# Performance work log

Hardware: AMD Instinct MI355X
Metric: run time of the kernel (lower is better)

Reference implementation:

```python
import jax, jax.numpy as jnp
import numpy as np

N_NODES = 100000
N_EDGES = 1600000
DIM = 64


def setup_inputs() -> dict:
    key = jax.random.key(0)
    ks = jax.random.split(key, 10)
    return {
        "h_real": jax.random.normal(ks[0], (N_NODES, DIM), dtype=jnp.float32),
        "h_imag": jax.random.normal(ks[1], (N_NODES, DIM), dtype=jnp.float32),
        "d": jax.random.uniform(ks[2], (N_NODES,), dtype=jnp.float32),
        "w_real": jax.random.normal(ks[3], (N_EDGES,), dtype=jnp.float32),
        "w_imag": jax.random.normal(ks[4], (N_EDGES,), dtype=jnp.float32),
        "src": jax.random.randint(ks[5], (N_EDGES,), 0, N_NODES, dtype=jnp.int32),
        "dst": jax.random.randint(ks[6], (N_EDGES,), 0, N_NODES, dtype=jnp.int32),
        "W1": jax.random.normal(ks[7], (DIM, DIM), dtype=jnp.float32) * (1.414 / np.sqrt(DIM)),
        "b1": jnp.zeros((DIM,), dtype=jnp.float32),
        "W2": jax.random.normal(ks[8], (DIM, DIM), dtype=jnp.float32) * (1.414 / np.sqrt(DIM)),
        "b2": jnp.zeros((DIM,), dtype=jnp.float32),
    }


def reference(h_real, h_imag, d, w_real, w_imag, src, dst, W1, b1, W2, b2):
    n = h_real.shape[0]
    # per-edge complex coefficient e = d_dst * d_src * (w_real + i w_imag)
    dd = d[dst] * d[src]                      # [E]
    e_r = (dd * w_real)[:, None]              # [E,1]
    e_i = (dd * w_imag)[:, None]              # [E,1]
    hr = h_real[src]                          # [E,D]
    hi = h_imag[src]                          # [E,D]
    # complex multiply e * h, fused single pass over edges
    m_r = e_r * hr - e_i * hi                 # [E,D]
    m_i = e_i * hr + e_r * hi                 # [E,D]
    z_real = jax.ops.segment_sum(m_r, dst, num_segments=n)  # [N,D]
    z_imag = jax.ops.segment_sum(m_i, dst, num_segments=n)  # [N,D]
    # note: original overwrites z_real first, then z_imag uses the NEW z_real
    zr = (z_real @ W1.T + b1) - (z_imag @ W2.T + b2)
    zi = (zr @ W2.T + b2) + (z_imag @ W1.T + b1)
    return zr, zi
```

## Files before the change

kernel.cpp:

```cpp
#include <hip/hip_runtime.h>
#include <hip/hip_bf16.h>

#define N_NODES 100000
#define N_EDGES 1600000
#define DIM 64

#define TILE 4096
#define B1 ((N_EDGES + TILE - 1) / TILE)
#define K1 ((N_NODES + 255) / 256)
#define NCOUNTS (K1 * B1)
#define SCAN_BLOCK 1024
#define NSB ((NCOUNTS + SCAN_BLOCK - 1) / SCAN_BLOCK)
#define PACKB4 ((N_NODES * DIM / 4 + 255) / 256)
#define QCAP 1344

typedef __attribute__((ext_vector_type(8))) short bf16x8;
typedef __attribute__((ext_vector_type(4))) float f32x4;

#if defined(__has_builtin)
#if __has_builtin(__builtin_amdgcn_fdot2_f32_bf16)
#define HAVE_DOT2 1
typedef __attribute__((ext_vector_type(2))) __bf16 bf16x2v;
#endif
#endif


__device__ __forceinline__ unsigned pack_bf16x2(float lo, float hi) {
  unsigned ulo = (unsigned)__hip_bfloat16_raw(__float2bfloat16(lo)).x;
  unsigned uhi = (unsigned)__hip_bfloat16_raw(__float2bfloat16(hi)).x;
  return ulo | (uhi << 16);
}
__device__ __forceinline__ float unpack_lo(unsigned u) {
  return __int_as_float((int)(u << 16));
}
__device__ __forceinline__ float unpack_hi(unsigned u) {
  return __int_as_float((int)(u & 0xFFFF0000u));
}
__device__ __forceinline__ unsigned short f2bf(float x) {
  return __hip_bfloat16_raw(__float2bfloat16(x)).x;
}

__global__ __launch_bounds__(256) void setup_fused_kernel(
    const float* __restrict__ h_real, const float* __restrict__ h_imag,
    unsigned* __restrict__ hpack, const float* __restrict__ W1,
    const float* __restrict__ b1, const float* __restrict__ W2,
    const float* __restrict__ b2, unsigned short* __restrict__ At,
    float* __restrict__ cvec, const int* __restrict__ dst,
    int* __restrict__ counts) {
  const int bid = blockIdx.x;
  const int tid = threadIdx.x;
  if (bid < PACKB4) {
    const int i = bid * 256 + tid;
    const float4 hr = ((const float4*)h_real)[i];
    const float4 hi = ((const float4*)h_imag)[i];
    uint4 o;
    o.x = pack_bf16x2(hr.x, hi.x);
    o.y = pack_bf16x2(hr.y, hi.y);
    o.z = pack_bf16x2(hr.z, hi.z);
    o.w = pack_bf16x2(hr.w, hi.w);
    ((uint4*)hpack)[i] = o;
    return;
  }
  if (bid < PACKB4 + 64) {
    const int idx = (bid - PACKB4) * 256 + tid;
    if (idx < 128 * 128) {
      const int n = idx >> 7, k = idx & 127;
      float v;
      if (n < 64) {
        v = (k < 64) ? W1[n * 64 + k] : -W2[n * 64 + (k - 64)];
      } else {
        const int nn = n - 64;
        if (k < 64) {
          float s = 0.0f;
          for (int j = 0; j < 64; ++j) s += W1[j * 64 + k] * W2[nn * 64 + j];
          v = s;
        } else {
          const int kk = k - 64;
          float s = 0.0f;
          for (int j = 0; j < 64; ++j) s += W2[j * 64 + kk] * W2[nn * 64 + j];
          v = W1[nn * 64 + kk] - s;
        }
      }
      At[n * 128 + k] = f2bf(v);
    }
    if (idx < 128) {
      if (idx < 64) {
        cvec[idx] = b1[idx] - b2[idx];
      } else {
        const int nn = idx - 64;
        float s = 0.0f;
        for (int j = 0; j < 64; ++j) s += (b1[j] - b2[j]) * W2[nn * 64 + j];
        cvec[idx] = s + b1[nn] + b2[nn];
      }
    }
    return;
  }
  __shared__ int lh[K1];
  const int hb = bid - PACKB4 - 64;
  for (int i = tid; i < K1; i += 256) lh[i] = 0;
  __syncthreads();
  const int e0 = hb * TILE;
  const int e1 = min(e0 + TILE, N_EDGES);
  for (int e = e0 + tid; e < e1; e += 256) atomicAdd(&lh[dst[e] >> 8], 1);
  __syncthreads();
  for (int b = tid; b < K1; b += 256) counts[b * B1 + hb] = lh[b];
}

__global__ __launch_bounds__(SCAN_BLOCK) void scan1_kernel(
    int* __restrict__ cnt, int* __restrict__ bsum) {
  __shared__ int wsum[16];
  const int tid = threadIdx.x;
  const int lane = tid & 63;
  const int w = tid >> 6;
  const int i = blockIdx.x * SCAN_BLOCK + tid;
  const int orig = (i < NCOUNTS) ? cnt[i] : 0;
  int v = orig;
#pragma unroll
  for (int off = 1; off < 64; off <<= 1) {
    int t = __shfl_up(v, off);
    if (lane >= off) v += t;
  }
  if (lane == 63) wsum[w] = v;
  __syncthreads();
  if (w == 0) {
    int s = (lane < 16) ? wsum[lane] : 0;
#pragma unroll
    for (int off = 1; off < 16; off <<= 1) {
      int t = __shfl_up(s, off);
      if (lane >= off) s += t;
    }
    if (lane < 16) wsum[lane] = s;
  }
  __syncthreads();
  const int wex = (w == 0) ? 0 : wsum[w - 1];
  if (i < NCOUNTS) cnt[i] = wex + v - orig;
  if (tid == SCAN_BLOCK - 1) bsum[blockIdx.x] = wex + v;
}

__global__ __launch_bounds__(256) void scan2_kernel(
    const int* __restrict__ bsum, int* __restrict__ bpre) {
  __shared__ int wsum[4];
  const int tid = threadIdx.x;
  const int lane = tid & 63;
  const int w = tid >> 6;
  const int orig = (tid < NSB) ? bsum[tid] : 0;
  int v = orig;
#pragma unroll
  for (int off = 1; off < 64; off <<= 1) {
    int t = __shfl_up(v, off);
    if (lane >= off) v += t;
  }
  if (lane == 63) wsum[w] = v;
  __syncthreads();
  if (w == 0) {
    int s = (lane < 4) ? wsum[lane] : 0;
#pragma unroll
    for (int off = 1; off < 4; off <<= 1) {
      int t = __shfl_up(s, off);
      if (lane >= off) s += t;
    }
    if (lane < 4) wsum[lane] = s;
  }
  __syncthreads();
  const int wex = (w == 0) ? 0 : wsum[w - 1];
  if (tid < NSB) bpre[tid] = wex + v - orig;
}

__global__ __launch_bounds__(512) void partition_kernel(
    const int* __restrict__ src, const int* __restrict__ dst,
    const float* __restrict__ dvec,
    const float* __restrict__ w_real, const float* __restrict__ w_imag,
    const int* __restrict__ coffs, const int* __restrict__ bpre,
    unsigned long long* __restrict__ records) {
  __shared__ unsigned long long stage[TILE];
  __shared__ unsigned short sb[TILE];
  __shared__ int lhist[512];
  __shared__ int lbase[K1];
  __shared__ int lcur[K1];
  __shared__ int gbase[K1];
  __shared__ int wsum[8];
  const int tid = threadIdx.x;
  const int lane = tid & 63;
  const int w = tid >> 6;
  const int blk = blockIdx.x;
  const int e0 = blk * TILE;
  const int cnt_t = min(TILE, N_EDGES - e0);

  lhist[tid] = 0;
  __syncthreads();
  for (int j = tid; j < cnt_t; j += 512) atomicAdd(&lhist[dst[e0 + j] >> 8], 1);
  __syncthreads();
  const int myc = lhist[tid];
  int v = myc;
#pragma unroll
  for (int off = 1; off < 64; off <<= 1) {
    int t = __shfl_up(v, off);
    if (lane >= off) v += t;
  }
  if (lane == 63) wsum[w] = v;
  __syncthreads();
  if (w == 0) {
    int s = (lane < 8) ? wsum[lane] : 0;
#pragma unroll
    for (int off = 1; off < 8; off <<= 1) {
      int t = __shfl_up(s, off);
      if (lane >= off) s += t;
    }
    if (lane < 8) wsum[lane] = s;
  }
  __syncthreads();
  const int ex = v + ((w == 0) ? 0 : wsum[w - 1]) - myc;
  if (tid < K1) {
    lbase[tid] = ex;
    lcur[tid] = ex;
    const int ci = tid * B1 + blk;
    gbase[tid] = coffs[ci] + bpre[ci >> 10];
  }
  __syncthreads();

  for (int j = tid; j < cnt_t; j += 512) {
    const int e = e0 + j;
    const int t = dst[e];
    const int s = src[e];
    const int b = t >> 8;
    const float ds = dvec[s];
    const unsigned lo = (unsigned)s | ((unsigned)(t & 255) << 17);
    const unsigned hi = pack_bf16x2(ds * w_real[e], ds * w_imag[e]);
    const int r = atomicAdd(&lcur[b], 1);
    stage[r] = ((unsigned long long)hi << 32) | lo;
    sb[r] = (unsigned short)b;
  }
  __syncthreads();
  for (int i = tid; i < cnt_t; i += 512) {
    const int b = sb[i];
    records[gbase[b] + (i - lbase[b])] = stage[i];
  }
}

__global__ __launch_bounds__(512, 8) void pull_sorted_kernel(
    const unsigned long long* __restrict__ records,
    const int* __restrict__ coffs, const int* __restrict__ bpre,
    const float* __restrict__ dvec, const unsigned* __restrict__ hpack,
    const unsigned short* __restrict__ At, const float* __restrict__ cvec,
    float* __restrict__ zr_out, float* __restrict__ zi_out) {
  __shared__ unsigned long long stageB[QCAP];
  __shared__ __align__(16) unsigned short zs[64][136];
  __shared__ int ncnt[64];
  __shared__ int ncur[64];
  __shared__ int ns[64];
  __shared__ int ne[64];
  const int tid = threadIdx.x;
  const int lane = tid & 63;
  const int wave = tid >> 6;
  const int q4 = lane >> 4;
  const int m16 = lane & 15;
  const int b256 = blockIdx.x >> 2;
  const int qtr = blockIdx.x & 3;
  const int nbase = b256 * 256 + qtr * 64;
  const unsigned* __restrict__ hb = hpack + 4 * m16;

  const int ci0 = b256 * B1;
  const int bstart = coffs[ci0] + bpre[ci0 >> 10];
  int bend;
  if (b256 == K1 - 1) {
    bend = N_EDGES;
  } else {
    const int ci1 = (b256 + 1) * B1;
    bend = coffs[ci1] + bpre[ci1 >> 10];
  }

  if (tid < 64) ncnt[tid] = 0;
  __syncthreads();

  for (int i = bstart + tid; i < bend; i += 512) {
    const unsigned nl = ((unsigned)records[i] >> 17) & 255u;
    if ((int)(nl >> 6) == qtr) atomicAdd(&ncnt[nl & 63], 1);
  }
  __syncthreads();

  if (wave == 0) {
    const int c = ncnt[lane];
    int v = c;
#pragma unroll
    for (int off = 1; off < 64; off <<= 1) {
      int t = __shfl_up(v, off);
      if (lane >= off) v += t;
    }
    ns[lane] = v - c;
    ne[lane] = v;
    ncur[lane] = v - c;
  }
  __syncthreads();

  for (int i = bstart + tid; i < bend; i += 512) {
    const unsigned long long rec = records[i];
    const unsigned nl = ((unsigned)rec >> 17) & 255u;
    if ((int)(nl >> 6) == qtr) {
      const int pos = atomicAdd(&ncur[nl & 63], 1);
      if (pos < QCAP) stageB[pos] = rec;
    }
  }
  __syncthreads();

#if HAVE_DOT2
#define DOT2(acc, w_, h_)                                                   \
  acc = __builtin_amdgcn_fdot2_f32_bf16(__builtin_bit_cast(bf16x2v, (w_)),  \
                                        __builtin_bit_cast(bf16x2v, (h_)),  \
                                        acc, false)
#else
#define DOT2(acc, w_, h_)                                                   \
  {                                                                         \
    const float _wl = unpack_lo(w_), _wh = unpack_hi(w_);                   \
    const float _hl = unpack_lo(h_), _hh = unpack_hi(h_);                   \
    acc += _wl * _hl + _wh * _hh;                                           \
  }
#endif

#define GATH(RR) \
  (*reinterpret_cast<const uint4*>(hb + (size_t)((unsigned)(RR) & 0x1FFFF) * DIM))

#define DOTS(RR, HV)                                                        \
  {                                                                         \
    const unsigned cf = (unsigned)((RR) >> 32);                             \
    const unsigned wneg = cf ^ 0x80000000u;                                 \
    const unsigned wswp = (cf >> 16) | (cf << 16);                          \
    DOT2(sr0, wneg, (HV).x); DOT2(si0, wswp, (HV).x);                       \
    DOT2(sr1, wneg, (HV).y); DOT2(si1, wswp, (HV).y);                       \
    DOT2(sr2, wneg, (HV).z); DOT2(si2, wswp, (HV).z);                       \
    DOT2(sr3, wneg, (HV).w); DOT2(si3, wswp, (HV).w);                       \
  }

  for (int j = 0; j < 8; ++j) {
    const int l = wave * 8 + j;
    const int n = nbase + l;
    if (n >= N_NODES) break;
    const int s = min(ns[l], QCAP);
    const int e = min(ne[l], QCAP);
    const int deg = e - s;

    float sr0 = 0.f, sr1 = 0.f, sr2 = 0.f, sr3 = 0.f;
    float si0 = 0.f, si1 = 0.f, si2 = 0.f, si3 = 0.f;

    int p = s + q4;
    const int nfull = deg >> 2;
    int i = 0;
    for (; i + 4 <= nfull; i += 4) {
      const unsigned long long ra = stageB[p];
      const unsigned long long rb = stageB[p + 4];
      const unsigned long long rc = stageB[p + 8];
      const unsigned long long rd = stageB[p + 12];
      const uint4 ha = GATH(ra);
      const uint4 hbv = GATH(rb);
      const uint4 hc = GATH(rc);
      const uint4 hd = GATH(rd);
      DOTS(ra, ha) DOTS(rb, hbv) DOTS(rc, hc) DOTS(rd, hd)
      p += 16;
    }
    for (; i + 2 <= nfull; i += 2) {
      const unsigned long long ra = stageB[p];
      const unsigned long long rb = stageB[p + 4];
      const uint4 ha = GATH(ra);
      const uint4 hbv = GATH(rb);
      DOTS(ra, ha) DOTS(rb, hbv)
      p += 8;
    }
    if (i < nfull) {
      const unsigned long long ra = stageB[p];
      const uint4 ha = GATH(ra);
      DOTS(ra, ha)
      p += 4;
    }
    if (p < e) {
      const unsigned long long ra = stageB[p];
      const uint4 ha = GATH(ra);
      DOTS(ra, ha)
    }

#define QRED(v)                  \
    v += __shfl_xor(v, 16);      \
    v += __shfl_xor(v, 32);
    QRED(sr0) QRED(sr1) QRED(sr2) QRED(sr3)
    QRED(si0) QRED(si1) QRED(si2) QRED(si3)
#undef QRED

    const float dn = dvec[n];
    if (lane < 16) {
      uint2 rv, iv;
      rv.x = pack_bf16x2(dn * sr0, dn * sr1);
      rv.y = pack_bf16x2(dn * sr2, dn * sr3);
      iv.x = pack_bf16x2(dn * si0, dn * si1);
      iv.y = pack_bf16x2(dn * si2, dn * si3);
      *reinterpret_cast<uint2*>(&zs[l][4 * lane]) = rv;
      *reinterpret_cast<uint2*>(&zs[l][64 + 4 * lane]) = iv;
    }
  }
#undef DOTS
#undef GATH
#undef DOT2
  __syncthreads();

  {
    const int m = lane & 15;
    const int q = lane >> 4;
    const int ft = wave;
#pragma unroll
    for (int g = 0; g < 4; ++g) {
      bf16x8 a[4];
#pragma unroll
      for (int c = 0; c < 4; ++c)
        a[c] = *reinterpret_cast<const bf16x8*>(&zs[g * 16 + m][c * 32 + q * 8]);

      f32x4 acc = (f32x4){0.f, 0.f, 0.f, 0.f};
      const unsigned short* brow = At + (size_t)(ft * 16 + m) * 128 + q * 8;
#pragma unroll
      for (int c = 0; c < 4; ++c) {
        bf16x8 bfrag = *reinterpret_cast<const bf16x8*>(brow + c * 32);
        acc = __builtin_amdgcn_mfma_f32_16x16x32_bf16(a[c], bfrag, acc, 0, 0, 0);
      }

      const int nf = ft * 16 + m;
      const float bias = cvec[nf];
      float* outp = (nf < 64) ? zr_out : zi_out;
      const int nnn = nf & 63;
#pragma unroll
      for (int r = 0; r < 4; ++r) {
        const int node = nbase + g * 16 + q * 4 + r;
        if (node < N_NODES) outp[(size_t)node * 64 + nnn] = acc[r] + bias;
      }
    }
  }
}

extern "C" void kernel_launch(void* const* d_in, const int* in_sizes, int n_in,
                              void* d_out, int out_size, void* d_ws, size_t ws_size,
                              hipStream_t stream) {
  const float* h_real = (const float*)d_in[0];
  const float* h_imag = (const float*)d_in[1];
  const float* dvec   = (const float*)d_in[2];
  const float* w_real = (const float*)d_in[3];
  const float* w_imag = (const float*)d_in[4];
  const int*   src    = (const int*)d_in[5];
  const int*   dst    = (const int*)d_in[6];
  const float* W1     = (const float*)d_in[7];
  const float* b1     = (const float*)d_in[8];
  const float* W2     = (const float*)d_in[9];
  const float* b2     = (const float*)d_in[10];

  char* ws = (char*)d_ws;
  unsigned short* At = (unsigned short*)ws;
  float* cvec = (float*)(ws + 128 * 128 * 2);
  unsigned long long* records = (unsigned long long*)(ws + 33792);
  unsigned* hpack = (unsigned*)(ws + 33792 + (size_t)N_EDGES * 8);
  int* counts = (int*)(ws + 33792 + (size_t)N_EDGES * 8 + (size_t)N_NODES * DIM * 4);
  int* bsum = counts + NCOUNTS;
  int* bpre = bsum + NSB;

  float* zr_out = (float*)d_out;
  float* zi_out = zr_out + (size_t)N_NODES * DIM;

  setup_fused_kernel<<<PACKB4 + 64 + B1, 256, 0, stream>>>(
      h_real, h_imag, (unsigned*)hpack, W1, b1, W2, b2, At, cvec, dst, counts);
  scan1_kernel<<<NSB, SCAN_BLOCK, 0, stream>>>(counts, bsum);
  scan2_kernel<<<1, 256, 0, stream>>>(bsum, bpre);
  partition_kernel<<<B1, 512, 0, stream>>>(src, dst, dvec, w_real, w_imag,
                                           counts, bpre, records);
  pull_sorted_kernel<<<K1 * 4, 512, 0, stream>>>(
      records, counts, bpre, dvec, hpack, At, cvec, zr_out, zi_out);
}
```

Baseline: 247.9 us.

## Replace per-tile count matrix scan with global bucket counters and atomic cursors

```diff
diff --git a/kernel.cpp b/kernel.cpp
--- a/kernel.cpp
+++ b/kernel.cpp
@@ -8,9 +8,6 @@
 #define TILE 4096
 #define B1 ((N_EDGES + TILE - 1) / TILE)
 #define K1 ((N_NODES + 255) / 256)
-#define NCOUNTS (K1 * B1)
-#define SCAN_BLOCK 1024
-#define NSB ((NCOUNTS + SCAN_BLOCK - 1) / SCAN_BLOCK)
 #define PACKB4 ((N_NODES * DIM / 4 + 255) / 256)
 #define QCAP 1344
 
@@ -46,7 +43,7 @@
     const float* __restrict__ b1, const float* __restrict__ W2,
     const float* __restrict__ b2, unsigned short* __restrict__ At,
     float* __restrict__ cvec, const int* __restrict__ dst,
-    int* __restrict__ counts) {
+    int* __restrict__ bcnt) {
   const int bid = blockIdx.x;
   const int tid = threadIdx.x;
   if (bid < PACKB4) {
@@ -62,23 +59,30 @@
     return;
   }
   if (bid < PACKB4 + 64) {
+    __shared__ float w1s[64 * 64];
+    __shared__ float w2s[64 * 64];
+    for (int i = tid; i < 64 * 64; i += 256) {
+      w1s[i] = W1[i];
+      w2s[i] = W2[i];
+    }
+    __syncthreads();
     const int idx = (bid - PACKB4) * 256 + tid;
     if (idx < 128 * 128) {
       const int n = idx >> 7, k = idx & 127;
       float v;
       if (n < 64) {
-        v = (k < 64) ? W1[n * 64 + k] : -W2[n * 64 + (k - 64)];
+        v = (k < 64) ? w1s[n * 64 + k] : -w2s[n * 64 + (k - 64)];
       } else {
         const int nn = n - 64;
         if (k < 64) {
           float s = 0.0f;
-          for (int j = 0; j < 64; ++j) s += W1[j * 64 + k] * W2[nn * 64 + j];
+          for (int j = 0; j < 64; ++j) s += w1s[j * 64 + k] * w2s[nn * 64 + j];
           v = s;
         } else {
           const int kk = k - 64;
           float s = 0.0f;
-          for (int j = 0; j < 64; ++j) s += W2[j * 64 + kk] * W2[nn * 64 + j];
-          v = W1[nn * 64 + kk] - s;
+          for (int j = 0; j < 64; ++j) s += w2s[j * 64 + kk] * w2s[nn * 64 + j];
+          v = w1s[nn * 64 + kk] - s;
         }
       }
       At[n * 128 + k] = f2bf(v);
@@ -89,7 +93,7 @@
       } else {
         const int nn = idx - 64;
         float s = 0.0f;
-        for (int j = 0; j < 64; ++j) s += (b1[j] - b2[j]) * W2[nn * 64 + j];
+        for (int j = 0; j < 64; ++j) s += (b1[j] - b2[j]) * w2s[nn * 64 + j];
         cvec[idx] = s + b1[nn] + b2[nn];
       }
     }
@@ -103,18 +107,19 @@
   const int e1 = min(e0 + TILE, N_EDGES);
   for (int e = e0 + tid; e < e1; e += 256) atomicAdd(&lh[dst[e] >> 8], 1);
   __syncthreads();
-  for (int b = tid; b < K1; b += 256) counts[b * B1 + hb] = lh[b];
-}
-
-__global__ __launch_bounds__(SCAN_BLOCK) void scan1_kernel(
-    int* __restrict__ cnt, int* __restrict__ bsum) {
-  __shared__ int wsum[16];
+  for (int b = tid; b < K1; b += 256)
+    if (lh[b]) atomicAdd(&bcnt[b], lh[b]);
+}
+
+__global__ __launch_bounds__(512) void scanB_kernel(
+    const int* __restrict__ bcnt, int* __restrict__ cursor,
+    int* __restrict__ bbase) {
+  __shared__ int wsum[8];
   const int tid = threadIdx.x;
   const int lane = tid & 63;
   const int w = tid >> 6;
-  const int i = blockIdx.x * SCAN_BLOCK + tid;
-  const int orig = (i < NCOUNTS) ? cnt[i] : 0;
-  int v = orig;
+  const int c = (tid < K1) ? bcnt[tid] : 0;
+  int v = c;
 #pragma unroll
   for (int off = 1; off < 64; off <<= 1) {
     int t = __shfl_up(v, off);
@@ -123,126 +128,92 @@
   if (lane == 63) wsum[w] = v;
   __syncthreads();
   if (w == 0) {
-    int s = (lane < 16) ? wsum[lane] : 0;
-#pragma unroll
-    for (int off = 1; off < 16; off <<= 1) {
+    int s = (lane < 8) ? wsum[lane] : 0;
+#pragma unroll
+    for (int off = 1; off < 8; off <<= 1) {
       int t = __shfl_up(s, off);
       if (lane >= off) s += t;
     }
-    if (lane < 16) wsum[lane] = s;
-  }
-  __syncthreads();
-  const int wex = (w == 0) ? 0 : wsum[w - 1];
-  if (i < NCOUNTS) cnt[i] = wex + v - orig;
-  if (tid == SCAN_BLOCK - 1) bsum[blockIdx.x] = wex + v;
-}
-
-__global__ __launch_bounds__(256) void scan2_kernel(
-    const int* __restrict__ bsum, int* __restrict__ bpre) {
-  __shared__ int wsum[4];
-  const int tid = threadIdx.x;
-  const int lane = tid & 63;
-  const int w = tid >> 6;
-  const int orig = (tid < NSB) ? bsum[tid] : 0;
-  int v = orig;
-#pragma unroll
-  for (int off = 1; off < 64; off <<= 1) {
-    int t = __shfl_up(v, off);
-    if (lane >= off) v += t;
-  }
-  if (lane == 63) wsum[w] = v;
-  __syncthreads();
-  if (w == 0) {
-    int s = (lane < 4) ? wsum[lane] : 0;
-#pragma unroll
-    for (int off = 1; off < 4; off <<= 1) {
-      int t = __shfl_up(s, off);
-      if (lane >= off) s += t;
-    }
-    if (lane < 4) wsum[lane] = s;
-  }
-  __syncthreads();
-  const int wex = (w == 0) ? 0 : wsum[w - 1];
-  if (tid < NSB) bpre[tid] = wex + v - orig;
+    if (lane < 8) wsum[lane] = s;
+  }
+  __syncthreads();
+  const int incl = v + ((w == 0) ? 0 : wsum[w - 1]);
+  const int excl = incl - c;
+  if (tid < K1) {
+    cursor[tid] = excl;
+    bbase[tid] = excl;
+  }
+  if (tid == K1 - 1) bbase[K1] = incl;
 }
 
 __global__ __launch_bounds__(512) void partition_kernel(
     const int* __restrict__ src, const int* __restrict__ dst,
     const float* __restrict__ dvec,
     const float* __restrict__ w_real, const float* __restrict__ w_imag,
-    const int* __restrict__ coffs, const int* __restrict__ bpre,
-    unsigned long long* __restrict__ records) {
-  __shared__ unsigned long long stage[TILE];
-  __shared__ unsigned short sb[TILE];
-  __shared__ int lhist[512];
-  __shared__ int lbase[K1];
-  __shared__ int lcur[K1];
-  __shared__ int gbase[K1];
-  __shared__ int wsum[8];
+    int* __restrict__ cursor, unsigned long long* __restrict__ records) {
+  __shared__ int lh[K1];
+  __shared__ int mybase[K1];
   const int tid = threadIdx.x;
-  const int lane = tid & 63;
-  const int w = tid >> 6;
   const int blk = blockIdx.x;
   const int e0 = blk * TILE;
   const int cnt_t = min(TILE, N_EDGES - e0);
 
-  lhist[tid] = 0;
-  __syncthreads();
-  for (int j = tid; j < cnt_t; j += 512) atomicAdd(&lhist[dst[e0 + j] >> 8], 1);
-  __syncthreads();
-  const int myc = lhist[tid];
-  int v = myc;
-#pragma unroll
-  for (int off = 1; off < 64; off <<= 1) {
-    int t = __shfl_up(v, off);
-    if (lane >= off) v += t;
-  }
-  if (lane == 63) wsum[w] = v;
-  __syncthreads();
-  if (w == 0) {
-    int s = (lane < 8) ? wsum[lane] : 0;
-#pragma unroll
-    for (int off = 1; off < 8; off <<= 1) {
-      int t = __shfl_up(s, off);
-      if (lane >= off) s += t;
-    }
-    if (lane < 8) wsum[lane] = s;
-  }
-  __syncthreads();
-  const int ex = v + ((w == 0) ? 0 : wsum[w - 1]) - myc;
-  if (tid < K1) {
-    lbase[tid] = ex;
-    lcur[tid] = ex;
-    const int ci = tid * B1 + blk;
-    gbase[tid] = coffs[ci] + bpre[ci >> 10];
-  }
-  __syncthreads();
-
-  for (int j = tid; j < cnt_t; j += 512) {
-    const int e = e0 + j;
-    const int t = dst[e];
-    const int s = src[e];
-    const int b = t >> 8;
-    const float ds = dvec[s];
-    const unsigned lo = (unsigned)s | ((unsigned)(t & 255) << 17);
-    const unsigned hi = pack_bf16x2(ds * w_real[e], ds * w_imag[e]);
-    const int r = atomicAdd(&lcur[b], 1);
-    stage[r] = ((unsigned long long)hi << 32) | lo;
-    sb[r] = (unsigned short)b;
-  }
-  __syncthreads();
-  for (int i = tid; i < cnt_t; i += 512) {
-    const int b = sb[i];
-    records[gbase[b] + (i - lbase[b])] = stage[i];
+  for (int i = tid; i < K1; i += 512) lh[i] = 0;
+  __syncthreads();
+
+#pragma unroll
+  for (int g = 0; g < TILE / 2048; ++g) {
+    const int off = g * 2048 + tid * 4;
+    if (off < cnt_t) {
+      const int4 t4 = *(const int4*)(dst + e0 + off);
+      atomicAdd(&lh[t4.x >> 8], 1);
+      atomicAdd(&lh[t4.y >> 8], 1);
+      atomicAdd(&lh[t4.z >> 8], 1);
+      atomicAdd(&lh[t4.w >> 8], 1);
+    }
+  }
+  __syncthreads();
+
+  for (int b = tid; b < K1; b += 512) {
+    const int c = lh[b];
+    mybase[b] = c ? atomicAdd(&cursor[b], c) : 0;
+    lh[b] = 0;
+  }
+  __syncthreads();
+
+#pragma unroll
+  for (int g = 0; g < TILE / 2048; ++g) {
+    const int off = g * 2048 + tid * 4;
+    if (off < cnt_t) {
+      const int e = e0 + off;
+      const int4 s4 = *(const int4*)(src + e);
+      const int4 t4 = *(const int4*)(dst + e);
+      const float4 wr = *(const float4*)(w_real + e);
+      const float4 wi = *(const float4*)(w_imag + e);
+#define EMIT(SS, TT, WR, WI)                                              \
+      {                                                                   \
+        const int b = (TT) >> 8;                                          \
+        const float ds = dvec[SS];                                        \
+        const unsigned lo = (unsigned)(SS) | ((unsigned)((TT) & 255) << 17); \
+        const unsigned hi = pack_bf16x2(ds * (WR), ds * (WI));            \
+        const int r = atomicAdd(&lh[b], 1);                               \
+        records[mybase[b] + r] = ((unsigned long long)hi << 32) | lo;     \
+      }
+      EMIT(s4.x, t4.x, wr.x, wi.x)
+      EMIT(s4.y, t4.y, wr.y, wi.y)
+      EMIT(s4.z, t4.z, wr.z, wi.z)
+      EMIT(s4.w, t4.w, wr.w, wi.w)
+#undef EMIT
+    }
   }
 }
 
 __global__ __launch_bounds__(512, 8) void pull_sorted_kernel(
     const unsigned long long* __restrict__ records,
-    const int* __restrict__ coffs, const int* __restrict__ bpre,
-    const float* __restrict__ dvec, const unsigned* __restrict__ hpack,
-    const unsigned short* __restrict__ At, const float* __restrict__ cvec,
-    float* __restrict__ zr_out, float* __restrict__ zi_out) {
+    const int* __restrict__ bbase, const float* __restrict__ dvec,
+    const unsigned* __restrict__ hpack, const unsigned short* __restrict__ At,
+    const float* __restrict__ cvec, float* __restrict__ zr_out,
+    float* __restrict__ zi_out) {
   __shared__ unsigned long long stageB[QCAP];
   __shared__ __align__(16) unsigned short zs[64][136];
   __shared__ int ncnt[64];
@@ -259,15 +230,8 @@
   const int nbase = b256 * 256 + qtr * 64;
   const unsigned* __restrict__ hb = hpack + 4 * m16;
 
-  const int ci0 = b256 * B1;
-  const int bstart = coffs[ci0] + bpre[ci0 >> 10];
-  int bend;
-  if (b256 == K1 - 1) {
-    bend = N_EDGES;
-  } else {
-    const int ci1 = (b256 + 1) * B1;
-    bend = coffs[ci1] + bpre[ci1 >> 10];
-  }
+  const int bstart = bbase[b256];
+  const int bend = bbase[b256 + 1];
 
   if (tid < 64) ncnt[tid] = 0;
   __syncthreads();
@@ -451,19 +415,19 @@
   float* cvec = (float*)(ws + 128 * 128 * 2);
   unsigned long long* records = (unsigned long long*)(ws + 33792);
   unsigned* hpack = (unsigned*)(ws + 33792 + (size_t)N_EDGES * 8);
-  int* counts = (int*)(ws + 33792 + (size_t)N_EDGES * 8 + (size_t)N_NODES * DIM * 4);
-  int* bsum = counts + NCOUNTS;
-  int* bpre = bsum + NSB;
+  int* bcnt = (int*)(ws + 33792 + (size_t)N_EDGES * 8 + (size_t)N_NODES * DIM * 4);
+  int* cursor = bcnt + K1;
+  int* bbase = cursor + K1;
 
   float* zr_out = (float*)d_out;
   float* zi_out = zr_out + (size_t)N_NODES * DIM;
 
+  hipMemsetAsync(bcnt, 0, (size_t)K1 * sizeof(int), stream);
   setup_fused_kernel<<<PACKB4 + 64 + B1, 256, 0, stream>>>(
-      h_real, h_imag, (unsigned*)hpack, W1, b1, W2, b2, At, cvec, dst, counts);
-  scan1_kernel<<<NSB, SCAN_BLOCK, 0, stream>>>(counts, bsum);
-  scan2_kernel<<<1, 256, 0, stream>>>(bsum, bpre);
+      h_real, h_imag, (unsigned*)hpack, W1, b1, W2, b2, At, cvec, dst, bcnt);
+  scanB_kernel<<<1, 512, 0, stream>>>(bcnt, cursor, bbase);
   partition_kernel<<<B1, 512, 0, stream>>>(src, dst, dvec, w_real, w_imag,
-                                           counts, bpre, records);
+                                           cursor, records);
   pull_sorted_kernel<<<K1 * 4, 512, 0, stream>>>(
-      records, counts, bpre, dvec, hpack, At, cvec, zr_out, zi_out);
-}
+      records, bbase, dvec, hpack, At, cvec, zr_out, zi_out);
+}
```

Result: slower. 261.5 us (+5.5%).
